# Kernel optimization log

Hardware: AMD Instinct MI355X
Metric: run time of the kernel (lower is better)

The kernel has to match this reference:

```python
import jax, jax.numpy as jnp
import numpy as np

N = 100000
E = 1600000

def setup_inputs() -> dict:
    key = jax.random.key(0)
    ks = jax.random.split(key, 8)
    x = jax.random.normal(ks[0], (N, 512), dtype=jnp.float32)
    edge_index = jax.random.randint(ks[1], (2, E), 0, N, dtype=jnp.int32)
    W1 = jax.random.normal(ks[2], (512, 64), dtype=jnp.float32) * (1.0 / np.sqrt(512))
    b1 = jnp.zeros((64,), dtype=jnp.float32)
    W2 = jax.random.normal(ks[3], (64, 32), dtype=jnp.float32) * (1.0 / np.sqrt(64))
    b2 = jnp.zeros((32,), dtype=jnp.float32)
    W3 = jax.random.normal(ks[4], (32, 4), dtype=jnp.float32) * (1.0 / np.sqrt(32))
    b3 = jnp.zeros((4,), dtype=jnp.float32)
    return {"x": x, "edge_index": edge_index, "W1": W1, "b1": b1,
            "W2": W2, "b2": b2, "W3": W3, "b3": b3}


def _gcn_norm(edge_index, n):
    # Add self-loops (fill_value=1), symmetric deg^{-1/2} normalization (PyG gcn_norm).
    loop = jnp.arange(n, dtype=edge_index.dtype)
    src = jnp.concatenate([edge_index[0], loop])
    dst = jnp.concatenate([edge_index[1], loop])
    w = jnp.ones((src.shape[0],), dtype=jnp.float32)
    deg = jax.ops.segment_sum(w, dst, num_segments=n)
    dinv = jnp.where(deg > 0, jax.lax.rsqrt(deg), 0.0)
    norm = dinv[src] * w * dinv[dst]
    return src, dst, norm


def _gcn_conv(x, W, b, src, dst, norm, n):
    h = x @ W                      # dense transform first (PyG GCNConv order)
    msg = h[src] * norm[:, None]   # gather + edge scaling
    out = jax.ops.segment_sum(msg, dst, num_segments=n)  # scatter-add aggregate
    return out + b


def reference(x, edge_index, W1, b1, W2, b2, W3, b3):
    n = x.shape[0]
    src, dst, norm = _gcn_norm(edge_index, n)  # cached=True: shared across layers
    h = jax.nn.relu(_gcn_conv(x, W1, b1, src, dst, norm, n))
    # dropout p=0.2 is identity in eval mode
    h = jax.nn.relu(_gcn_conv(h, W2, b2, src, dst, norm, n))
    # dropout p=0.4 is identity in eval mode
    out = _gcn_conv(h, W3, b3, src, dst, norm, n)
    return out
```

## Files before the change

kernel.cpp:

```cpp
#include <hip/hip_runtime.h>


typedef __attribute__((ext_vector_type(8))) short short8;
typedef __attribute__((ext_vector_type(4))) float floatx4;

#define NBUK_MAX 512
#define SC_EDGES 6144
#define HIST_EDGES 8192

__device__ __forceinline__ unsigned f2bf_bits(float f) {
    unsigned u = __float_as_uint(f);
    return (u + 0x7fffu + ((u >> 16) & 1u)) >> 16;
}
__device__ __forceinline__ float bf_bits2f(unsigned b) {
    return __uint_as_float(b << 16);
}

__global__ __launch_bounds__(256) void zero_i32(int* p, int n) {
    int i = blockIdx.x * 256 + threadIdx.x;
    if (i < n) p[i] = 0;
}

__global__ __launch_bounds__(512) void bucket_hist(const int* __restrict__ dst,
                                                   int* __restrict__ buckcnt,
                                                   int e, int shift, int nbuk) {
    __shared__ int hist[NBUK_MAX];
    int t = threadIdx.x;
    for (int i = t; i < nbuk; i += 512) hist[i] = 0;
    __syncthreads();
    long long base = (long long)blockIdx.x * HIST_EDGES;
#pragma unroll
    for (int j = 0; j < HIST_EDGES / 512; j++) {
        long long i = base + j * 512 + t;
        if (i < e) atomicAdd(&hist[dst[i] >> shift], 1);
    }
    __syncthreads();
    for (int i = t; i < nbuk; i += 512)
        if (hist[i] > 0) atomicAdd(&buckcnt[i], hist[i]);
}

__global__ __launch_bounds__(512) void bucket_scan(const int* __restrict__ buckcnt,
                                                   int* __restrict__ boff,
                                                   int* __restrict__ buckfill,
                                                   int* __restrict__ rowptr,
                                                   int nbuk, int n, int e) {
    __shared__ int sc[512];
    int t = threadIdx.x;
    int v = (t < nbuk) ? buckcnt[t] : 0;
    sc[t] = v;
    __syncthreads();
    for (int off = 1; off < 512; off <<= 1) {
        int u = (t >= off) ? sc[t - off] : 0;
        __syncthreads();
        sc[t] += u;
        __syncthreads();
    }
    int excl = sc[t] - v;
    if (t < nbuk) {
        boff[t] = excl;
        buckfill[t] = excl;
    }
    if (t == 0) {
        boff[nbuk] = e;
        rowptr[n] = e;
    }
}

__global__ __launch_bounds__(512) void bucket_scatter(const int* __restrict__ src,
                                                      const int* __restrict__ dst,
                                                      int* __restrict__ buckfill,
                                                      int2* __restrict__ colpair,
                                                      int e, int shift, int nbuk) {
    __shared__ int hist[NBUK_MAX];
    __shared__ int lscan[NBUK_MAX];
    __shared__ int fillL[NBUK_MAX];
    __shared__ int baseG[NBUK_MAX];
    __shared__ int2 stage[SC_EDGES];
    int t = threadIdx.x;
    for (int i = t; i < nbuk; i += 512) hist[i] = 0;
    __syncthreads();
    long long base = (long long)blockIdx.x * SC_EDGES;
#pragma unroll
    for (int j = 0; j < SC_EDGES / 512; j++) {
        long long i = base + j * 512 + t;
        if (i < e) atomicAdd(&hist[dst[i] >> shift], 1);
    }
    __syncthreads();
    int v = (t < nbuk) ? hist[t] : 0;
    lscan[t] = v;
    __syncthreads();
    for (int off = 1; off < 512; off <<= 1) {
        int u = (t >= off) ? lscan[t - off] : 0;
        __syncthreads();
        lscan[t] += u;
        __syncthreads();
    }
    int excl = lscan[t] - v;
    lscan[t] = excl;
    fillL[t] = excl;
    if (t < nbuk && v > 0) baseG[t] = atomicAdd(&buckfill[t], v);
    __syncthreads();
#pragma unroll
    for (int j = 0; j < SC_EDGES / 512; j++) {
        long long i = base + j * 512 + t;
        if (i < e) {
            int d = dst[i];
            int s = src[i];
            int p = atomicAdd(&fillL[d >> shift], 1);
            stage[p] = make_int2(s, d);
        }
    }
    __syncthreads();
    long long rem = (long long)e - base;
    int cnt = (rem < SC_EDGES) ? (int)rem : SC_EDGES;
    for (int k = t; k < cnt; k += 512) {
        int2 pr = stage[k];
        int b = pr.y >> shift;
        colpair[baseG[b] + (k - lscan[b])] = pr;
    }
}

__global__ __launch_bounds__(512) void csr_build(const int2* __restrict__ colpair,
                                                 const int* __restrict__ boff,
                                                 int* __restrict__ rowptr,
                                                 float* __restrict__ dinv,
                                                 int* __restrict__ colidx,
                                                 int n, int shift) {
    __shared__ int degl[NBUK_MAX];
    __shared__ int lsc[NBUK_MAX];
    __shared__ int fill[NBUK_MAX];
    int t = threadIdx.x;
    int bn = 1 << shift;
    int node0 = blockIdx.x << shift;
    int e0 = boff[blockIdx.x];
    int e1 = boff[blockIdx.x + 1];
    if (t < bn) degl[t] = 0;
    __syncthreads();
    for (int i = e0 + t; i < e1; i += 512)
        atomicAdd(&degl[colpair[i].y - node0], 1);
    __syncthreads();
    int v = (t < bn) ? degl[t] : 0;
    lsc[t] = v;
    __syncthreads();
    for (int off = 1; off < 512; off <<= 1) {
        int u = (t >= off) ? lsc[t - off] : 0;
        __syncthreads();
        lsc[t] += u;
        __syncthreads();
    }
    int excl = lsc[t] - v;
    int node = node0 + t;
    if (t < bn && node < n) {
        rowptr[node] = e0 + excl;
        dinv[node] = rsqrtf((float)(v + 1));
    }
    fill[t] = e0 + excl;
    __syncthreads();
    for (int i = e0 + t; i < e1; i += 512) {
        int2 pr = colpair[i];
        int p = atomicAdd(&fill[pr.y - node0], 1);
        colidx[p] = pr.x;
    }
}

__global__ __launch_bounds__(256) void w1_split(const float* __restrict__ W1,
                                                short* __restrict__ whi,
                                                short* __restrict__ wlo) {
    int idx = blockIdx.x * 256 + threadIdx.x;
    int k = idx >> 6;
    int nn = idx & 63;
    float v = W1[idx];
    unsigned hb = f2bf_bits(v);
    float lof = v - bf_bits2f(hb);
    unsigned lb = f2bf_bits(lof);
    int kc = k >> 5, rem = k & 31, quad = rem >> 3, j = rem & 7;
    int ct = nn >> 4, l = nn & 15;
    int lane = quad * 16 + l;
    int addr = ((ct * 16 + kc) * 64 + lane) * 8 + j;
    whi[addr] = (short)hb;
    wlo[addr] = (short)lb;
}

__global__ __launch_bounds__(256) void transform1_mfma(const float* __restrict__ x,
                                                       const short* __restrict__ whi,
                                                       const short* __restrict__ wlo,
                                                       const float* __restrict__ dinv,
                                                       float* __restrict__ h1, int n) {
    __shared__ float xs[64 * 36];
    const int t = threadIdx.x;
    const int w = t >> 6;
    const int lane = t & 63;
    const int quad = lane >> 4;
    const int row0 = blockIdx.x * 64;
    const int mrow = w * 16 + (lane & 15);
    floatx4 acc[4] = {{0.f, 0.f, 0.f, 0.f}, {0.f, 0.f, 0.f, 0.f},
                      {0.f, 0.f, 0.f, 0.f}, {0.f, 0.f, 0.f, 0.f}};

    for (int kc = 0; kc < 16; kc++) {
        __syncthreads();
#pragma unroll
        for (int i = 0; i < 2; i++) {
            int c = t + i * 256;
            int m = c >> 3;
            int koff = (c & 7) << 2;
            int grow = row0 + m;
            float4 v = make_float4(0.f, 0.f, 0.f, 0.f);
            if (grow < n) v = *(const float4*)&x[(size_t)grow * 512 + kc * 32 + koff];
            *(float4*)&xs[m * 36 + koff] = v;
        }
        __syncthreads();
        float a[8];
        *(float4*)&a[0] = *(const float4*)&xs[mrow * 36 + quad * 8];
        *(float4*)&a[4] = *(const float4*)&xs[mrow * 36 + quad * 8 + 4];
        short8 ahi, alo;
#pragma unroll
        for (int j = 0; j < 8; j++) {
            unsigned hb = f2bf_bits(a[j]);
            float lof = a[j] - bf_bits2f(hb);
            unsigned lb = f2bf_bits(lof);
            ahi[j] = (short)hb;
            alo[j] = (short)lb;
        }
        const int base = (kc * 64 + lane) * 8;
#pragma unroll
        for (int ct = 0; ct < 4; ct++) {
            short8 bhi = *(const short8*)&whi[ct * 8192 + base];
            short8 blo = *(const short8*)&wlo[ct * 8192 + base];
            acc[ct] = __builtin_amdgcn_mfma_f32_16x16x32_bf16(ahi, bhi, acc[ct], 0, 0, 0);
            acc[ct] = __builtin_amdgcn_mfma_f32_16x16x32_bf16(alo, bhi, acc[ct], 0, 0, 0);
            acc[ct] = __builtin_amdgcn_mfma_f32_16x16x32_bf16(ahi, blo, acc[ct], 0, 0, 0);
        }
    }
#pragma unroll
    for (int r = 0; r < 4; r++) {
        int grow = row0 + w * 16 + quad * 4 + r;
        if (grow < n) {
            float s = dinv[grow];
#pragma unroll
            for (int ct = 0; ct < 4; ct++) {
                h1[(size_t)grow * 64 + ct * 16 + (lane & 15)] = acc[ct][r] * s;
            }
        }
    }
}

__global__ __launch_bounds__(256) void transform2(const float* __restrict__ g1,
                                                  const float* __restrict__ W2,
                                                  const float* __restrict__ dinv,
                                                  float* __restrict__ h2, int n) {
    __shared__ float rows[32 * 68];
    __shared__ float W2s[64 * 32];
    int t = threadIdx.x;
    int row0 = blockIdx.x * 32;
#pragma unroll
    for (int i = 0; i < 2; i++) {
        int c = t + i * 256;
        int r = c >> 4, k4 = (c & 15) << 2;
        int grow = row0 + r;
        float4 v = make_float4(0.f, 0.f, 0.f, 0.f);
        if (grow < n) v = *(const float4*)&g1[(size_t)grow * 64 + k4];
        *(float4*)&rows[r * 68 + k4] = v;
    }
#pragma unroll
    for (int i = 0; i < 2; i++) {
        int c = t + i * 256;
        *(float4*)&W2s[c * 4] = *(const float4*)&W2[c * 4];
    }
    __syncthreads();
    int lr = t >> 3;
    int c4 = (t & 7) * 4;
    int row = row0 + lr;
    float a0 = 0.f, a1 = 0.f, a2 = 0.f, a3 = 0.f;
#pragma unroll
    for (int k4 = 0; k4 < 64; k4 += 4) {
        float4 a = *(const float4*)&rows[lr * 68 + k4];
        float4 w0 = *(const float4*)&W2s[(k4 + 0) * 32 + c4];
        float4 w1 = *(const float4*)&W2s[(k4 + 1) * 32 + c4];
        float4 w2 = *(const float4*)&W2s[(k4 + 2) * 32 + c4];
        float4 w3 = *(const float4*)&W2s[(k4 + 3) * 32 + c4];
        a0 += a.x * w0.x + a.y * w1.x + a.z * w2.x + a.w * w3.x;
        a1 += a.x * w0.y + a.y * w1.y + a.z * w2.y + a.w * w3.y;
        a2 += a.x * w0.z + a.y * w1.z + a.z * w2.z + a.w * w3.z;
        a3 += a.x * w0.w + a.y * w1.w + a.z * w2.w + a.w * w3.w;
    }
    if (row < n) {
        float s = dinv[row];
        float4 o = make_float4(a0 * s, a1 * s, a2 * s, a3 * s);
        *(float4*)&h2[(size_t)row * 32 + c4] = o;
    }
}

__global__ __launch_bounds__(256) void transform3(const float* __restrict__ g2,
                                                  const float* __restrict__ W3,
                                                  const float* __restrict__ dinv,
                                                  float* __restrict__ h3, int n) {
    __shared__ float W3s[128];
    int t = threadIdx.x;
    if (t < 128) W3s[t] = W3[t];
    __syncthreads();
    int row = blockIdx.x * 256 + t;
    if (row >= n) return;
    float a0 = 0.f, a1 = 0.f, a2 = 0.f, a3 = 0.f;
    const float4* rp = (const float4*)&g2[(size_t)row * 32];
#pragma unroll
    for (int kk = 0; kk < 8; kk++) {
        float4 v = rp[kk];
        float4 w0 = *(const float4*)&W3s[(4 * kk + 0) * 4];
        float4 w1 = *(const float4*)&W3s[(4 * kk + 1) * 4];
        float4 w2 = *(const float4*)&W3s[(4 * kk + 2) * 4];
        float4 w3 = *(const float4*)&W3s[(4 * kk + 3) * 4];
        a0 += v.x * w0.x + v.y * w1.x + v.z * w2.x + v.w * w3.x;
        a1 += v.x * w0.y + v.y * w1.y + v.z * w2.y + v.w * w3.y;
        a2 += v.x * w0.z + v.y * w1.z + v.z * w2.z + v.w * w3.z;
        a3 += v.x * w0.w + v.y * w1.w + v.z * w2.w + v.w * w3.w;
    }
    float s = dinv[row];
    float4 o = make_float4(a0 * s, a1 * s, a2 * s, a3 * s);
    *(float4*)&h3[(size_t)row * 4] = o;
}

template <int F, bool RELU>
__global__ __launch_bounds__(256) void aggregate_ilp(const float* __restrict__ h,
                                                     const int* __restrict__ rowptr,
                                                     const int* __restrict__ colidx,
                                                     const float* __restrict__ dinv,
                                                     const float* __restrict__ bias,
                                                     float* __restrict__ out, int n) {
    int tid = blockIdx.x * 256 + threadIdx.x;
    int node = tid / F;
    int f = tid & (F - 1);
    if (node >= n) return;
    int r0 = rowptr[node], r1 = rowptr[node + 1];
    float acc0 = h[(size_t)node * F + f];
    float acc1 = 0.f, acc2 = 0.f, acc3 = 0.f;
    float acc4 = 0.f, acc5 = 0.f, acc6 = 0.f, acc7 = 0.f;
    int j = r0;
    for (; j + 7 < r1; j += 8) {
        int c0 = colidx[j + 0];
        int c1 = colidx[j + 1];
        int c2 = colidx[j + 2];
        int c3 = colidx[j + 3];
        int c4 = colidx[j + 4];
        int c5 = colidx[j + 5];
        int c6 = colidx[j + 6];
        int c7 = colidx[j + 7];
        acc0 += h[(size_t)c0 * F + f];
        acc1 += h[(size_t)c1 * F + f];
        acc2 += h[(size_t)c2 * F + f];
        acc3 += h[(size_t)c3 * F + f];
        acc4 += h[(size_t)c4 * F + f];
        acc5 += h[(size_t)c5 * F + f];
        acc6 += h[(size_t)c6 * F + f];
        acc7 += h[(size_t)c7 * F + f];
    }
    for (; j < r1; j++) {
        acc0 += h[(size_t)colidx[j] * F + f];
    }
    float acc = ((acc0 + acc1) + (acc2 + acc3)) + ((acc4 + acc5) + (acc6 + acc7));
    float v = dinv[node] * acc + bias[f];
    if (RELU) v = fmaxf(v, 0.f);
    out[(size_t)node * F + f] = v;
}

extern "C" void kernel_launch(void* const* d_in, const int* in_sizes, int n_in,
                              void* d_out, int out_size, void* d_ws, size_t ws_size,
                              hipStream_t stream) {
    const float* x  = (const float*)d_in[0];
    const int*   ei = (const int*)d_in[1];
    const float* W1 = (const float*)d_in[2];
    const float* b1 = (const float*)d_in[3];
    const float* W2 = (const float*)d_in[4];
    const float* b2 = (const float*)d_in[5];
    const float* W3 = (const float*)d_in[6];
    const float* b3 = (const float*)d_in[7];
    const int n = in_sizes[0] / 512;
    const int e = in_sizes[1] / 2;
    const int* src = ei;
    const int* dst = ei + e;
    float* out = (float*)d_out;

    char* p = (char*)d_ws;
    auto alloc = [&](size_t bytes) {
        void* r = (void*)p;
        p += (bytes + 255) & ~(size_t)255;
        return r;
    };
    int*   buckcnt  = (int*)alloc((size_t)NBUK_MAX * 4);
    int*   boff     = (int*)alloc((size_t)(NBUK_MAX + 1) * 4);
    int*   buckfill = (int*)alloc((size_t)NBUK_MAX * 4);
    int*   rowptr   = (int*)alloc((size_t)(n + 1) * 4);
    int*   colidx   = (int*)alloc((size_t)e * 4);
    float* dinv     = (float*)alloc((size_t)n * 4);
    short* whi      = (short*)alloc((size_t)32768 * 2);
    short* wlo      = (short*)alloc((size_t)32768 * 2);
    float* bufA     = (float*)alloc((size_t)n * 64 * 4);
    float* bufB     = (float*)alloc((size_t)n * 64 * 4);
    int2*  colpair  = (int2*)bufA;

    int shift = 8;
    while (((n + (1 << shift) - 1) >> shift) > NBUK_MAX) shift++;
    const int nbuk = (n + (1 << shift) - 1) >> shift;

    const int HB = (int)(((long long)e + HIST_EDGES - 1) / HIST_EDGES);
    const int SB = (int)(((long long)e + SC_EDGES - 1) / SC_EDGES);

    zero_i32<<<dim3((nbuk + 255) / 256), dim3(256), 0, stream>>>(buckcnt, nbuk);
    bucket_hist<<<dim3(HB), dim3(512), 0, stream>>>(dst, buckcnt, e, shift, nbuk);
    bucket_scan<<<dim3(1), dim3(512), 0, stream>>>(buckcnt, boff, buckfill, rowptr, nbuk, n, e);
    bucket_scatter<<<dim3(SB), dim3(512), 0, stream>>>(src, dst, buckfill, colpair, e, shift, nbuk);
    csr_build<<<dim3(nbuk), dim3(512), 0, stream>>>(colpair, boff, rowptr, dinv, colidx, n, shift);
    w1_split<<<dim3(128), dim3(256), 0, stream>>>(W1, whi, wlo);

    transform1_mfma<<<dim3((n + 63) / 64), dim3(256), 0, stream>>>(x, whi, wlo, dinv, bufA, n);
    aggregate_ilp<64, true><<<dim3((int)(((size_t)n * 64 + 255) / 256)), dim3(256), 0, stream>>>(bufA, rowptr, colidx, dinv, b1, bufB, n);
    transform2<<<dim3((n + 31) / 32), dim3(256), 0, stream>>>(bufB, W2, dinv, bufA, n);
    aggregate_ilp<32, true><<<dim3((int)(((size_t)n * 32 + 255) / 256)), dim3(256), 0, stream>>>(bufA, rowptr, colidx, dinv, b2, bufB, n);
    transform3<<<dim3((n + 255) / 256), dim3(256), 0, stream>>>(bufB, W3, dinv, bufA, n);
    aggregate_ilp<4, false><<<dim3((int)(((size_t)n * 4 + 255) / 256)), dim3(256), 0, stream>>>(bufA, rowptr, colidx, dinv, b3, out, n);
}
```

Measured before the change: 510.1 us.

## Load x directly to registers in transform1 and fuse layer-3 transform into aggregate

transform1 now loads each lane's A-fragment of x straight from global memory into registers, prefetching one k-chunk ahead, instead of staging tiles through shared memory with two barriers per chunk. The second-layer aggregation now also applies ReLU and the 32x4 W3 projection, reducing across the 32 feature lanes with xor shuffles, which removes the separate transform3 kernel and its round trip of the 32-wide activations. The direct loads give each lane a 32-byte strided access pattern instead of cooperative coalesced loads, which may lower memory efficiency for the large x read.

```diff
diff --git a/kernel.cpp b/kernel.cpp
--- a/kernel.cpp
+++ b/kernel.cpp
@@ -186,32 +186,28 @@
                                                        const short* __restrict__ wlo,
                                                        const float* __restrict__ dinv,
                                                        float* __restrict__ h1, int n) {
-    __shared__ float xs[64 * 36];
     const int t = threadIdx.x;
     const int w = t >> 6;
     const int lane = t & 63;
     const int quad = lane >> 4;
     const int row0 = blockIdx.x * 64;
-    const int mrow = w * 16 + (lane & 15);
+    const int grow = row0 + w * 16 + (lane & 15);
+    const int growc = (grow < n) ? grow : (n - 1);
+    const float* xp = x + (size_t)growc * 512 + quad * 8;
+
     floatx4 acc[4] = {{0.f, 0.f, 0.f, 0.f}, {0.f, 0.f, 0.f, 0.f},
                       {0.f, 0.f, 0.f, 0.f}, {0.f, 0.f, 0.f, 0.f}};
 
+    float4 a0 = *(const float4*)&xp[0];
+    float4 a1 = *(const float4*)&xp[4];
+
     for (int kc = 0; kc < 16; kc++) {
-        __syncthreads();
-#pragma unroll
-        for (int i = 0; i < 2; i++) {
-            int c = t + i * 256;
-            int m = c >> 3;
-            int koff = (c & 7) << 2;
-            int grow = row0 + m;
-            float4 v = make_float4(0.f, 0.f, 0.f, 0.f);
-            if (grow < n) v = *(const float4*)&x[(size_t)grow * 512 + kc * 32 + koff];
-            *(float4*)&xs[m * 36 + koff] = v;
+        float4 n0, n1;
+        if (kc < 15) {
+            n0 = *(const float4*)&xp[(kc + 1) * 32 + 0];
+            n1 = *(const float4*)&xp[(kc + 1) * 32 + 4];
         }
-        __syncthreads();
-        float a[8];
-        *(float4*)&a[0] = *(const float4*)&xs[mrow * 36 + quad * 8];
-        *(float4*)&a[4] = *(const float4*)&xs[mrow * 36 + quad * 8 + 4];
+        float a[8] = {a0.x, a0.y, a0.z, a0.w, a1.x, a1.y, a1.z, a1.w};
         short8 ahi, alo;
 #pragma unroll
         for (int j = 0; j < 8; j++) {
@@ -230,15 +226,17 @@
             acc[ct] = __builtin_amdgcn_mfma_f32_16x16x32_bf16(alo, bhi, acc[ct], 0, 0, 0);
             acc[ct] = __builtin_amdgcn_mfma_f32_16x16x32_bf16(ahi, blo, acc[ct], 0, 0, 0);
         }
+        a0 = n0;
+        a1 = n1;
     }
 #pragma unroll
     for (int r = 0; r < 4; r++) {
-        int grow = row0 + w * 16 + quad * 4 + r;
-        if (grow < n) {
-            float s = dinv[grow];
+        int orow = row0 + w * 16 + quad * 4 + r;
+        if (orow < n) {
+            float s = dinv[orow];
 #pragma unroll
             for (int ct = 0; ct < 4; ct++) {
-                h1[(size_t)grow * 64 + ct * 16 + (lane & 15)] = acc[ct][r] * s;
+                h1[(size_t)orow * 64 + ct * 16 + (lane & 15)] = acc[ct][r] * s;
             }
         }
     }
@@ -288,35 +286,6 @@
         float4 o = make_float4(a0 * s, a1 * s, a2 * s, a3 * s);
         *(float4*)&h2[(size_t)row * 32 + c4] = o;
     }
-}
-
-__global__ __launch_bounds__(256) void transform3(const float* __restrict__ g2,
-                                                  const float* __restrict__ W3,
-                                                  const float* __restrict__ dinv,
-                                                  float* __restrict__ h3, int n) {
-    __shared__ float W3s[128];
-    int t = threadIdx.x;
-    if (t < 128) W3s[t] = W3[t];
-    __syncthreads();
-    int row = blockIdx.x * 256 + t;
-    if (row >= n) return;
-    float a0 = 0.f, a1 = 0.f, a2 = 0.f, a3 = 0.f;
-    const float4* rp = (const float4*)&g2[(size_t)row * 32];
-#pragma unroll
-    for (int kk = 0; kk < 8; kk++) {
-        float4 v = rp[kk];
-        float4 w0 = *(const float4*)&W3s[(4 * kk + 0) * 4];
-        float4 w1 = *(const float4*)&W3s[(4 * kk + 1) * 4];
-        float4 w2 = *(const float4*)&W3s[(4 * kk + 2) * 4];
-        float4 w3 = *(const float4*)&W3s[(4 * kk + 3) * 4];
-        a0 += v.x * w0.x + v.y * w1.x + v.z * w2.x + v.w * w3.x;
-        a1 += v.x * w0.y + v.y * w1.y + v.z * w2.y + v.w * w3.y;
-        a2 += v.x * w0.z + v.y * w1.z + v.z * w2.z + v.w * w3.z;
-        a3 += v.x * w0.w + v.y * w1.w + v.z * w2.w + v.w * w3.w;
-    }
-    float s = dinv[row];
-    float4 o = make_float4(a0 * s, a1 * s, a2 * s, a3 * s);
-    *(float4*)&h3[(size_t)row * 4] = o;
 }
 
 template <int F, bool RELU>
@@ -362,6 +331,62 @@
     out[(size_t)node * F + f] = v;
 }
 
+__global__ __launch_bounds__(256) void aggregate32_t3(const float* __restrict__ h,
+                                                      const int* __restrict__ rowptr,
+                                                      const int* __restrict__ colidx,
+                                                      const float* __restrict__ dinv,
+                                                      const float* __restrict__ bias,
+                                                      const float* __restrict__ W3,
+                                                      float* __restrict__ h3, int n) {
+    int tid = blockIdx.x * 256 + threadIdx.x;
+    int node = tid >> 5;
+    int f = tid & 31;
+    if (node >= n) return;
+    int r0 = rowptr[node], r1 = rowptr[node + 1];
+    float acc0 = h[(size_t)node * 32 + f];
+    float acc1 = 0.f, acc2 = 0.f, acc3 = 0.f;
+    float acc4 = 0.f, acc5 = 0.f, acc6 = 0.f, acc7 = 0.f;
+    int j = r0;
+    for (; j + 7 < r1; j += 8) {
+        int c0 = colidx[j + 0];
+        int c1 = colidx[j + 1];
+        int c2 = colidx[j + 2];
+        int c3 = colidx[j + 3];
+        int c4 = colidx[j + 4];
+        int c5 = colidx[j + 5];
+        int c6 = colidx[j + 6];
+        int c7 = colidx[j + 7];
+        acc0 += h[(size_t)c0 * 32 + f];
+        acc1 += h[(size_t)c1 * 32 + f];
+        acc2 += h[(size_t)c2 * 32 + f];
+        acc3 += h[(size_t)c3 * 32 + f];
+        acc4 += h[(size_t)c4 * 32 + f];
+        acc5 += h[(size_t)c5 * 32 + f];
+        acc6 += h[(size_t)c6 * 32 + f];
+        acc7 += h[(size_t)c7 * 32 + f];
+    }
+    for (; j < r1; j++) {
+        acc0 += h[(size_t)colidx[j] * 32 + f];
+    }
+    float acc = ((acc0 + acc1) + (acc2 + acc3)) + ((acc4 + acc5) + (acc6 + acc7));
+    float dn = dinv[node];
+    float v = dn * acc + bias[f];
+    v = fmaxf(v, 0.f);
+    float4 wr = *(const float4*)&W3[f * 4];
+    float p0 = v * wr.x, p1 = v * wr.y, p2 = v * wr.z, p3 = v * wr.w;
+#pragma unroll
+    for (int m = 16; m >= 1; m >>= 1) {
+        p0 += __shfl_xor(p0, m);
+        p1 += __shfl_xor(p1, m);
+        p2 += __shfl_xor(p2, m);
+        p3 += __shfl_xor(p3, m);
+    }
+    if (f < 4) {
+        float r = (f == 0) ? p0 : (f == 1) ? p1 : (f == 2) ? p2 : p3;
+        h3[(size_t)node * 4 + f] = dn * r;
+    }
+}
+
 extern "C" void kernel_launch(void* const* d_in, const int* in_sizes, int n_in,
                               void* d_out, int out_size, void* d_ws, size_t ws_size,
                               hipStream_t stream) {
@@ -414,7 +439,6 @@
     transform1_mfma<<<dim3((n + 63) / 64), dim3(256), 0, stream>>>(x, whi, wlo, dinv, bufA, n);
     aggregate_ilp<64, true><<<dim3((int)(((size_t)n * 64 + 255) / 256)), dim3(256), 0, stream>>>(bufA, rowptr, colidx, dinv, b1, bufB, n);
     transform2<<<dim3((n + 31) / 32), dim3(256), 0, stream>>>(bufB, W2, dinv, bufA, n);
-    aggregate_ilp<32, true><<<dim3((int)(((size_t)n * 32 + 255) / 256)), dim3(256), 0, stream>>>(bufA, rowptr, colidx, dinv, b2, bufB, n);
-    transform3<<<dim3((n + 255) / 256), dim3(256), 0, stream>>>(bufB, W3, dinv, bufA, n);
-    aggregate_ilp<4, false><<<dim3((int)(((size_t)n * 4 + 255) / 256)), dim3(256), 0, stream>>>(bufA, rowptr, colidx, dinv, b3, out, n);
-}
+    aggregate32_t3<<<dim3((int)(((size_t)n * 32 + 255) / 256)), dim3(256), 0, stream>>>(bufA, rowptr, colidx, dinv, b2, W3, bufB, n);
+    aggregate_ilp<4, false><<<dim3((int)(((size_t)n * 4 + 255) / 256)), dim3(256), 0, stream>>>(bufB, rowptr, colidx, dinv, b3, out, n);
+}
```

Measured after the change: 517.1 us. No clear change (+1.4%).

## Use wave-per-node aggregation with float4 gathers and fuse layer-3 transform

Applied to the files above, without the earlier changes.

Replaces the thread-per-feature aggregation kernels with wave-per-node kernels. Lanes split edges into slots and read float4 feature chunks, then reduce across slots with cross-lane shuffles. The layer-2 aggregation now also applies the 32x4 W3 transform and dinv scaling directly, which removes the separate transform3 kernel and one intermediate round trip to memory. The scatter edge chunk size is also halved. The layer-4 aggregation leaves most lanes idle for low-degree nodes, and the shuffle reductions add fixed cost per node.

```diff
diff --git a/kernel.cpp b/kernel.cpp
--- a/kernel.cpp
+++ b/kernel.cpp
@@ -5,7 +5,7 @@
 typedef __attribute__((ext_vector_type(4))) float floatx4;
 
 #define NBUK_MAX 512
-#define SC_EDGES 6144
+#define SC_EDGES 3072
 #define HIST_EDGES 8192
 
 __device__ __forceinline__ unsigned f2bf_bits(float f) {
@@ -290,76 +290,143 @@
     }
 }
 
-__global__ __launch_bounds__(256) void transform3(const float* __restrict__ g2,
-                                                  const float* __restrict__ W3,
+__device__ __forceinline__ void f4acc(float4& a, const float4 b) {
+    a.x += b.x; a.y += b.y; a.z += b.z; a.w += b.w;
+}
+__device__ __forceinline__ void f4shflxor(float4& a, int m) {
+    a.x += __shfl_xor(a.x, m);
+    a.y += __shfl_xor(a.y, m);
+    a.z += __shfl_xor(a.z, m);
+    a.w += __shfl_xor(a.w, m);
+}
+
+__global__ __launch_bounds__(256) void agg64_wave(const float* __restrict__ h,
+                                                  const int* __restrict__ rowptr,
+                                                  const int* __restrict__ colidx,
                                                   const float* __restrict__ dinv,
-                                                  float* __restrict__ h3, int n) {
-    __shared__ float W3s[128];
-    int t = threadIdx.x;
-    if (t < 128) W3s[t] = W3[t];
-    __syncthreads();
-    int row = blockIdx.x * 256 + t;
-    if (row >= n) return;
-    float a0 = 0.f, a1 = 0.f, a2 = 0.f, a3 = 0.f;
-    const float4* rp = (const float4*)&g2[(size_t)row * 32];
-#pragma unroll
-    for (int kk = 0; kk < 8; kk++) {
-        float4 v = rp[kk];
-        float4 w0 = *(const float4*)&W3s[(4 * kk + 0) * 4];
-        float4 w1 = *(const float4*)&W3s[(4 * kk + 1) * 4];
-        float4 w2 = *(const float4*)&W3s[(4 * kk + 2) * 4];
-        float4 w3 = *(const float4*)&W3s[(4 * kk + 3) * 4];
-        a0 += v.x * w0.x + v.y * w1.x + v.z * w2.x + v.w * w3.x;
-        a1 += v.x * w0.y + v.y * w1.y + v.z * w2.y + v.w * w3.y;
-        a2 += v.x * w0.z + v.y * w1.z + v.z * w2.z + v.w * w3.z;
-        a3 += v.x * w0.w + v.y * w1.w + v.z * w2.w + v.w * w3.w;
-    }
-    float s = dinv[row];
-    float4 o = make_float4(a0 * s, a1 * s, a2 * s, a3 * s);
-    *(float4*)&h3[(size_t)row * 4] = o;
-}
-
-template <int F, bool RELU>
-__global__ __launch_bounds__(256) void aggregate_ilp(const float* __restrict__ h,
-                                                     const int* __restrict__ rowptr,
-                                                     const int* __restrict__ colidx,
-                                                     const float* __restrict__ dinv,
-                                                     const float* __restrict__ bias,
-                                                     float* __restrict__ out, int n) {
-    int tid = blockIdx.x * 256 + threadIdx.x;
-    int node = tid / F;
-    int f = tid & (F - 1);
+                                                  const float* __restrict__ bias,
+                                                  float* __restrict__ out, int n) {
+    int node = (blockIdx.x * 256 + threadIdx.x) >> 6;
     if (node >= n) return;
+    int lane = threadIdx.x & 63;
+    int eslot = lane >> 4;
+    int fq = (lane & 15) << 2;
     int r0 = rowptr[node], r1 = rowptr[node + 1];
-    float acc0 = h[(size_t)node * F + f];
-    float acc1 = 0.f, acc2 = 0.f, acc3 = 0.f;
-    float acc4 = 0.f, acc5 = 0.f, acc6 = 0.f, acc7 = 0.f;
+    float4 z = make_float4(0.f, 0.f, 0.f, 0.f);
+    float4 a0 = z, a1 = z, a2 = z, a3 = z;
+    if (eslot == 0) a0 = *(const float4*)&h[(size_t)node * 64 + fq];
     int j = r0;
-    for (; j + 7 < r1; j += 8) {
-        int c0 = colidx[j + 0];
-        int c1 = colidx[j + 1];
-        int c2 = colidx[j + 2];
-        int c3 = colidx[j + 3];
-        int c4 = colidx[j + 4];
-        int c5 = colidx[j + 5];
-        int c6 = colidx[j + 6];
-        int c7 = colidx[j + 7];
-        acc0 += h[(size_t)c0 * F + f];
-        acc1 += h[(size_t)c1 * F + f];
-        acc2 += h[(size_t)c2 * F + f];
-        acc3 += h[(size_t)c3 * F + f];
-        acc4 += h[(size_t)c4 * F + f];
-        acc5 += h[(size_t)c5 * F + f];
-        acc6 += h[(size_t)c6 * F + f];
-        acc7 += h[(size_t)c7 * F + f];
-    }
-    for (; j < r1; j++) {
-        acc0 += h[(size_t)colidx[j] * F + f];
-    }
-    float acc = ((acc0 + acc1) + (acc2 + acc3)) + ((acc4 + acc5) + (acc6 + acc7));
-    float v = dinv[node] * acc + bias[f];
-    if (RELU) v = fmaxf(v, 0.f);
-    out[(size_t)node * F + f] = v;
+    for (; j + 15 < r1; j += 16) {
+        int c0 = colidx[j + eslot];
+        int c1 = colidx[j + 4 + eslot];
+        int c2 = colidx[j + 8 + eslot];
+        int c3 = colidx[j + 12 + eslot];
+        f4acc(a0, *(const float4*)&h[(size_t)c0 * 64 + fq]);
+        f4acc(a1, *(const float4*)&h[(size_t)c1 * 64 + fq]);
+        f4acc(a2, *(const float4*)&h[(size_t)c2 * 64 + fq]);
+        f4acc(a3, *(const float4*)&h[(size_t)c3 * 64 + fq]);
+    }
+    {
+        int e0 = j + eslot, e1 = j + 4 + eslot, e2 = j + 8 + eslot, e3 = j + 12 + eslot;
+        if (e0 < r1) f4acc(a0, *(const float4*)&h[(size_t)colidx[e0] * 64 + fq]);
+        if (e1 < r1) f4acc(a1, *(const float4*)&h[(size_t)colidx[e1] * 64 + fq]);
+        if (e2 < r1) f4acc(a2, *(const float4*)&h[(size_t)colidx[e2] * 64 + fq]);
+        if (e3 < r1) f4acc(a3, *(const float4*)&h[(size_t)colidx[e3] * 64 + fq]);
+    }
+    f4acc(a0, a1); f4acc(a2, a3); f4acc(a0, a2);
+    f4shflxor(a0, 16);
+    f4shflxor(a0, 32);
+    if (eslot == 0) {
+        float dn = dinv[node];
+        float4 b = *(const float4*)&bias[fq];
+        float4 v = make_float4(fmaxf(dn * a0.x + b.x, 0.f), fmaxf(dn * a0.y + b.y, 0.f),
+                               fmaxf(dn * a0.z + b.z, 0.f), fmaxf(dn * a0.w + b.w, 0.f));
+        *(float4*)&out[(size_t)node * 64 + fq] = v;
+    }
+}
+
+__global__ __launch_bounds__(256) void agg32_t3(const float* __restrict__ h,
+                                                const int* __restrict__ rowptr,
+                                                const int* __restrict__ colidx,
+                                                const float* __restrict__ dinv,
+                                                const float* __restrict__ bias,
+                                                const float* __restrict__ W3,
+                                                float* __restrict__ h3, int n) {
+    int node = (blockIdx.x * 256 + threadIdx.x) >> 6;
+    if (node >= n) return;
+    int lane = threadIdx.x & 63;
+    int eslot = lane >> 3;
+    int fq = (lane & 7) << 2;
+    int r0 = rowptr[node], r1 = rowptr[node + 1];
+    float4 z = make_float4(0.f, 0.f, 0.f, 0.f);
+    float4 a0 = z, a1 = z;
+    if (eslot == 0) a0 = *(const float4*)&h[(size_t)node * 32 + fq];
+    int j = r0;
+    for (; j + 15 < r1; j += 16) {
+        int c0 = colidx[j + eslot];
+        int c1 = colidx[j + 8 + eslot];
+        f4acc(a0, *(const float4*)&h[(size_t)c0 * 32 + fq]);
+        f4acc(a1, *(const float4*)&h[(size_t)c1 * 32 + fq]);
+    }
+    {
+        int e0 = j + eslot, e1 = j + 8 + eslot;
+        if (e0 < r1) f4acc(a0, *(const float4*)&h[(size_t)colidx[e0] * 32 + fq]);
+        if (e1 < r1) f4acc(a1, *(const float4*)&h[(size_t)colidx[e1] * 32 + fq]);
+    }
+    f4acc(a0, a1);
+    f4shflxor(a0, 8);
+    f4shflxor(a0, 16);
+    f4shflxor(a0, 32);
+    float dn = dinv[node];
+    float4 b = *(const float4*)&bias[fq];
+    float4 g = make_float4(fmaxf(dn * a0.x + b.x, 0.f), fmaxf(dn * a0.y + b.y, 0.f),
+                           fmaxf(dn * a0.z + b.z, 0.f), fmaxf(dn * a0.w + b.w, 0.f));
+    float4 w0 = *(const float4*)&W3[(fq + 0) * 4];
+    float4 w1 = *(const float4*)&W3[(fq + 1) * 4];
+    float4 w2 = *(const float4*)&W3[(fq + 2) * 4];
+    float4 w3 = *(const float4*)&W3[(fq + 3) * 4];
+    float4 p = make_float4(g.x * w0.x + g.y * w1.x + g.z * w2.x + g.w * w3.x,
+                           g.x * w0.y + g.y * w1.y + g.z * w2.y + g.w * w3.y,
+                           g.x * w0.z + g.y * w1.z + g.z * w2.z + g.w * w3.z,
+                           g.x * w0.w + g.y * w1.w + g.z * w2.w + g.w * w3.w);
+    f4shflxor(p, 1);
+    f4shflxor(p, 2);
+    f4shflxor(p, 4);
+    if (lane == 0) {
+        *(float4*)&h3[(size_t)node * 4] =
+            make_float4(dn * p.x, dn * p.y, dn * p.z, dn * p.w);
+    }
+}
+
+__global__ __launch_bounds__(256) void agg4_wave(const float* __restrict__ h,
+                                                 const int* __restrict__ rowptr,
+                                                 const int* __restrict__ colidx,
+                                                 const float* __restrict__ dinv,
+                                                 const float* __restrict__ bias,
+                                                 float* __restrict__ out, int n) {
+    int node = (blockIdx.x * 256 + threadIdx.x) >> 6;
+    if (node >= n) return;
+    int lane = threadIdx.x & 63;
+    int eslot = lane >> 2;
+    int f = lane & 3;
+    int r0 = rowptr[node], r1 = rowptr[node + 1];
+    float a0 = (eslot == 0) ? h[(size_t)node * 4 + f] : 0.f;
+    float a1 = 0.f;
+    int j = r0;
+    for (; j + 15 < r1; j += 16) {
+        int c = colidx[j + eslot];
+        a0 += h[(size_t)c * 4 + f];
+    }
+    {
+        int e = j + eslot;
+        if (e < r1) a1 += h[(size_t)colidx[e] * 4 + f];
+    }
+    float s = a0 + a1;
+    s += __shfl_xor(s, 4);
+    s += __shfl_xor(s, 8);
+    s += __shfl_xor(s, 16);
+    s += __shfl_xor(s, 32);
+    if (eslot == 0) out[(size_t)node * 4 + f] = dinv[node] * s + bias[f];
 }
 
 extern "C" void kernel_launch(void* const* d_in, const int* in_sizes, int n_in,
@@ -403,6 +470,7 @@
 
     const int HB = (int)(((long long)e + HIST_EDGES - 1) / HIST_EDGES);
     const int SB = (int)(((long long)e + SC_EDGES - 1) / SC_EDGES);
+    const int WPN = (n + 3) / 4;
 
     zero_i32<<<dim3((nbuk + 255) / 256), dim3(256), 0, stream>>>(buckcnt, nbuk);
     bucket_hist<<<dim3(HB), dim3(512), 0, stream>>>(dst, buckcnt, e, shift, nbuk);
@@ -412,9 +480,8 @@
     w1_split<<<dim3(128), dim3(256), 0, stream>>>(W1, whi, wlo);
 
     transform1_mfma<<<dim3((n + 63) / 64), dim3(256), 0, stream>>>(x, whi, wlo, dinv, bufA, n);
-    aggregate_ilp<64, true><<<dim3((int)(((size_t)n * 64 + 255) / 256)), dim3(256), 0, stream>>>(bufA, rowptr, colidx, dinv, b1, bufB, n);
+    agg64_wave<<<dim3(WPN), dim3(256), 0, stream>>>(bufA, rowptr, colidx, dinv, b1, bufB, n);
     transform2<<<dim3((n + 31) / 32), dim3(256), 0, stream>>>(bufB, W2, dinv, bufA, n);
-    aggregate_ilp<32, true><<<dim3((int)(((size_t)n * 32 + 255) / 256)), dim3(256), 0, stream>>>(bufA, rowptr, colidx, dinv, b2, bufB, n);
-    transform3<<<dim3((n + 255) / 256), dim3(256), 0, stream>>>(bufB, W3, dinv, bufA, n);
-    aggregate_ilp<4, false><<<dim3((int)(((size_t)n * 4 + 255) / 256)), dim3(256), 0, stream>>>(bufA, rowptr, colidx, dinv, b3, out, n);
-}
+    agg32_t3<<<dim3(WPN), dim3(256), 0, stream>>>(bufA, rowptr, colidx, dinv, b2, W3, bufB, n);
+    agg4_wave<<<dim3(WPN), dim3(256), 0, stream>>>(bufB, rowptr, colidx, dinv, b3, out, n);
+}
```

Result: no change. 516.0 us (+1.2%).
